# Kernel optimization log

Hardware: AMD Instinct MI355X
Metric: run time of the kernel (lower is better)

The kernel has to match this reference:

```python
import jax, jax.numpy as jnp
from jax import lax
import numpy as np

FACTOR = 2
KERNEL = 3  # conv kernel size (odd)
DN = ('NCDHW', 'OIDHW', 'NCDHW')


def _setup_fir_kernel():
    # resample_kernel = (1,3,3,1); separable outer product, normalized, * factor**3 gain
    k1 = jnp.asarray([1.0, 3.0, 3.0, 1.0], dtype=jnp.float32)
    k = jnp.einsum('i,j,k->ijk', k1, k1, k1)
    k = k / jnp.sum(k)
    return k * (FACTOR ** 3)  # [4,4,4]


def _upfirdn3d_1x1(x, k, pad0, pad1):
    # upfirdn3d with up=down=1: pad then depthwise-correlate with flipped FIR kernel
    # (torch code runs F.conv3d with torch.flip(kernel)).
    n, c = x.shape[0], x.shape[1]
    xp = jnp.pad(x, ((0, 0), (0, 0), (pad0, pad1), (pad0, pad1), (pad0, pad1)))
    kf = jnp.flip(k).astype(x.dtype)  # flip all 3 spatial axes
    w = jnp.broadcast_to(kf[None, None], (c, 1) + k.shape)  # depthwise [C,1,4,4,4]
    return lax.conv_general_dilated(xp, w, (1, 1, 1), 'VALID',
                                    dimension_numbers=DN,
                                    feature_group_count=c)


def _upsample_conv_3d(x, weight):
    # Equivalent of upsample_conv_3d(x, w, k=(1,3,3,1), factor=2):
    # torch flips the weight and feeds conv_transpose3d(stride=2); the flip and
    # the implicit transpose-flip cancel, so it equals an lhs-dilated correlation
    # with the ORIGINAL weight, padded by (k-1) on each side (output_padding=0).
    k = _setup_fir_kernel()
    p = k.shape[0] - FACTOR - (KERNEL - 1)  # = 0
    pad_lo, pad_hi = (p + 1) // 2 + FACTOR - 1, p // 2 + 1  # = (1, 1)
    y = lax.conv_general_dilated(
        x, weight.astype(x.dtype), (1, 1, 1),
        padding=[(KERNEL - 1, KERNEL - 1)] * 3,
        lhs_dilation=(FACTOR, FACTOR, FACTOR),
        dimension_numbers=DN)  # [N, outC, 33, 33, 33]
    return _upfirdn3d_1x1(y, k, pad_lo, pad_hi)  # [N, outC, 32, 32, 32]


def setup_inputs() -> dict:
    key = jax.random.key(0)
    k1, k2, k3 = jax.random.split(key, 3)
    x = jax.random.normal(k1, (8, 256, 16, 16, 16), dtype=jnp.float32)
    weight = jax.random.normal(k2, (128, 256, 3, 3, 3), dtype=jnp.float32) * 0.05
    bias = jax.random.normal(k3, (128,), dtype=jnp.float32) * 0.05
    return {"x": x, "weight": weight, "bias": bias}


def reference(x, weight, bias):
    y = _upsample_conv_3d(x, weight)
    return y + bias.reshape(1, -1, 1, 1, 1)
```

## Files before the change

kernel.cpp:

```cpp
#include <hip/hip_runtime.h>
#include <string.h>

typedef __attribute__((ext_vector_type(4))) float f32x4;
typedef __attribute__((ext_vector_type(8))) _Float16 f16x8;
typedef unsigned short u16;
typedef unsigned int   u32;

#define NBATCH 8
#define ICN 256
#define OCN 128
#define VOLP 36432
#define WRE 884736
#define XTE 8388608
#define ZBF 4096
#define S1POOL 43520

__host__ __device__ constexpr int cls_yoff2(int c){
  return (c==0)?0:(c==1)?5168:(c==2)?9792:(c==3)?14416:
         (c==4)?18768:(c==5)?23632:(c==6)?27984:32336;
}
__host__ __device__ constexpr int cls_nxyp(int c){
  return ((c&3)==0)?304:((c&3)==3)?256:272;
}

__device__ __forceinline__ u16 f2h(float v){
  _Float16 h = (_Float16)v;
  u16 u; memcpy(&u, &h, 2);
  return u;
}
__device__ __forceinline__ float h2f(u16 u){
  _Float16 h; memcpy(&h, &u, 2);
  return (float)h;
}

#define GLOAD16(gp, lp)                                                        \
  __builtin_amdgcn_global_load_lds(                                            \
      (const __attribute__((address_space(1))) void*)(gp),                     \
      (__attribute__((address_space(3))) void*)(lp), 16, 0, 0)

__global__ __launch_bounds__(256) void prep_w(const float* __restrict__ w,
                                              u16* __restrict__ wh,
                                              float* __restrict__ zb){
  if (blockIdx.x < 16) zb[blockIdx.x*256 + threadIdx.x] = 0.f;
  int idx = blockIdx.x*256 + threadIdx.x;
  int e = idx&7, ln=(idx>>3)&63, og=(idx>>9)&7, icc=(idx>>12)&7, tt=idx>>15;
  int oc = og*16 + (ln&15);
  int ic = icc*32 + ((ln>>4)&3)*8 + e;
  const int toffs[8] = {0,8,12,16,18,22,24,26};
  const int tcnt[8]  = {8,4,4,2,4,2,2,1};
  int c=0, t=0;
  #pragma unroll
  for (int cc=0; cc<8; ++cc)
    if (tt>=toffs[cc] && tt<toffs[cc]+tcnt[cc]){ c=cc; t=tt-toffs[cc]; }
  int ez=c>>2, ey=(c>>1)&1, ex=c&1;
  int ty=2-ey, tx=2-ex;
  int ax=t%tx, ay=(t/tx)%ty, az=t/(tx*ty);
  int qz = ez?1:(az?2:0), qy = ey?1:(ay?2:0), qx = ex?1:(ax?2:0);
  wh[idx] = f2h(w[((size_t)oc*ICN + ic)*27 + (qz*3+qy)*3+qx]);
}

__global__ __launch_bounds__(256) void prep_x(const float* __restrict__ x,
                                              u16* __restrict__ xh){
  __shared__ u16 tile[256*33];
  const int tid = threadIdx.x;
  const int b = blockIdx.x;
  const int n = b >> 7, icc = (b >> 4) & 7, pc = b & 15;
  const float* xb = x + ((size_t)(n*256 + icc*32))*4096 + pc*256;
  #pragma unroll 4
  for (int r = 0; r < 32; ++r)
    tile[tid*33 + r] = f2h(xb[(size_t)r*4096 + tid]);
  __syncthreads();
  u16* ob = xh + ((size_t)(n*8 + icc))*131072 + pc*8192;
  #pragma unroll
  for (int j = 0; j < 4; ++j){
    int c = j*256 + tid;
    int p = c >> 2, il8 = (c & 3)*8;
    ushort4 lo, hi;
    lo.x = tile[p*33+il8+0]; lo.y = tile[p*33+il8+1];
    lo.z = tile[p*33+il8+2]; lo.w = tile[p*33+il8+3];
    hi.x = tile[p*33+il8+4]; hi.y = tile[p*33+il8+5];
    hi.z = tile[p*33+il8+6]; hi.w = tile[p*33+il8+7];
    *(ushort4*)&ob[c*8]     = lo;
    *(ushort4*)&ob[c*8 + 4] = hi;
  }
}

#define S1_ISSUE(BUFBYTE, ICC0, AZV)                                           \
  {                                                                            \
    const int iccs_ = wv >> 1;                                                 \
    _Pragma("unroll")                                                          \
    for (int j_=0; j_<6; ++j_){                                                \
      const int r_ = j_*64 + ln;                                               \
      if (r_ < 340){                                                           \
        const int s_ = wv*340 + r_;                                            \
        const int in_ = s_ - iccs_*680;                                        \
        const int icg_ = in_&3, pos_ = in_>>2;                                 \
        const int xi_ = pos_%17, yi_ = pos_/17;                                \
        const int zc_ = EZ ? mz : (mz-1+(AZV));                                \
        const int yc_ = my0 + yi_ + (EY-1);                                    \
        const int xc_ = xi_ + (EX-1);                                          \
        const bool inb_ = (u32)zc_<16u && (u32)yc_<16u && (u32)xc_<16u;        \
        const size_t g_ = nbase + (size_t)((ICC0)+iccs_)*131072                \
                        + (size_t)((zc_*256+yc_*16+xc_)*32 + icg_*8);          \
        const u16* gh_ = inb_ ? (xh+g_) : zb16;                                \
        char* lh_ = pool + (BUFBYTE) + s_*16;                                  \
        GLOAD16(gh_, lh_);                                                     \
      }                                                                        \
    }                                                                          \
  }

template<int EZ,int EY,int EX>
__device__ __forceinline__ void s1body(char* pool,
                                       const u16* __restrict__ xh,
                                       const u16* __restrict__ wh,
                                       const u16* __restrict__ zb16,
                                       u16* __restrict__ yd, int n0, int mt, int mz, int nl, int tid)
{
  constexpr int TZ=2-EZ, TY=2-EY, TX=2-EX;
  constexpr int DX=17-EX;
  constexpr int DY=17-EY;
  constexpr int NXY=DY*DX;
  constexpr int CLS = EZ*4+EY*2+EX;
  constexpr int YOFF = cls_yoff2(CLS);
  constexpr int NXYP = cls_nxyp(CLS);
  constexpr int W27 = (CLS==0)?0:(CLS==1)?8:(CLS==2)?12:(CLS==3)?16:
                      (CLS==4)?18:(CLS==5)?22:(CLS==6)?24:26;
  constexpr int NST = TZ*4;
  u16* AsU = (u16*)pool;

  const int wv=tid>>6, ln=tid&63;
  const int mhalf = wv&1, ochalf = wv>>1;
  const int my0=(mt*128)/DX;

  int posA[4];
  #pragma unroll
  for (int fi=0; fi<4; ++fi){
    int m = mt*128 + mhalf*64 + fi*16 + (ln&15);
    if (m > NXY-1) m = NXY-1;
    int my=m/DX, mx=m-my*DX;
    posA[fi] = ((my-my0)*17 + mx)*32 + (ln>>4)*8;
  }

  f32x4 acc[4][4];
  #pragma unroll
  for (int i=0;i<4;++i)
    #pragma unroll
    for (int j=0;j<4;++j) acc[i][j]=(f32x4){0.f,0.f,0.f,0.f};

  const size_t nbase = (size_t)(n0+nl)*(ICN*4096);

  S1_ISSUE(0, 0, 0);

  int st = 0;
  #pragma unroll 1
  for (int ip=0; ip<4; ++ip){
    #pragma unroll
    for (int az=0; az<TZ; ++az){
      const int cur = st & 1;
      const bool have_next = (st+1) < NST;
      if (have_next){
        const int nip = (az+1<TZ)?ip:(ip+1);
        const int naz = (az+1<TZ)?(az+1):0;
        S1_ISSUE((cur^1)*21760, nip*2, naz);
        asm volatile("s_waitcnt vmcnt(6)" ::: "memory");
      } else {
        asm volatile("s_waitcnt vmcnt(0)" ::: "memory");
      }
      asm volatile("s_barrier" ::: "memory");
      const int curo = cur*10880;

      __builtin_amdgcn_s_setprio(1);
      #pragma unroll
      for (int k=0; k<2; ++k){
        const int icc = ip*2 + k;
        #pragma unroll
        for (int ay=0; ay<TY; ++ay)
        #pragma unroll
        for (int ax=0; ax<TX; ++ax){
          const int t = (az*TY+ay)*TX+ax;
          const int toff = (ay*17+ax)*32;
          f16x8 ah[4];
          #pragma unroll
          for (int fi=0; fi<4; ++fi)
            ah[fi] = *(const f16x8*)&AsU[curo + k*5440 + posA[fi]+toff];
          const u16* bp = wh + (size_t)(((W27+t)*8+icc)*8)*512 + (ochalf*4)*512 + ln*8;
          f16x8 bh[4];
          #pragma unroll
          for (int og=0; og<4; ++og) bh[og] = *(const f16x8*)(bp + og*512);
          #pragma unroll
          for (int fi=0; fi<4; ++fi)
            #pragma unroll
            for (int og=0; og<4; ++og)
              acc[fi][og] = __builtin_amdgcn_mfma_f32_16x16x32_f16(ah[fi], bh[og], acc[fi][og],0,0,0);
        }
      }
      __builtin_amdgcn_s_setprio(0);
      asm volatile("s_barrier" ::: "memory");
      ++st;
    }
  }

  float* tr = (float*)pool + wv*(64*33);
  #pragma unroll
  for (int pass=0; pass<2; ++pass){
    #pragma unroll
    for (int fi=0; fi<2; ++fi)
      #pragma unroll
      for (int og=0; og<4; ++og)
        #pragma unroll
        for (int j=0; j<4; ++j)
          tr[(og*16+(ln&15))*33 + fi*16 + (ln>>4)*4 + j] = acc[pass*2+fi][og][j];
    int m = mt*128 + mhalf*64 + pass*32 + (ln&31);
    bool valid = m < NXY;
    size_t lbase = (size_t)YOFF + (size_t)mz*NXYP + (valid ? m : 0);
    #pragma unroll 4
    for (int i=0; i<32; ++i){
      int r = 2*i + (ln>>5);
      u16 v = f2h(tr[r*33 + (ln&31)]);
      int oc = ochalf*64 + r;
      if (valid)
        __builtin_nontemporal_store(v, yd + (size_t)(nl*128 + oc)*VOLP + lbase);
    }
  }
}

__global__ __launch_bounds__(256,3) void stage1f(const u16* __restrict__ xh,
                                                 const u16* __restrict__ wh,
                                                 const u16* __restrict__ zb16,
                                                 u16* __restrict__ yd, int n0){
  __shared__ __align__(16) char pool[S1POOL];
  int bid = blockIdx.x, nl, tid = threadIdx.x;
  if (gridDim.z == 1){ nl = bid & 7; bid >>= 3; }
  else               { nl = blockIdx.z; }
  int mz, sub;
  if (bid < 352){ mz = bid/22; sub = bid - mz*22; }
  else          { mz = 16;     sub = bid - 352;   }
  if      (sub <  3) s1body<0,0,0>(pool,xh,wh,zb16,yd,n0,sub   ,mz,nl,tid);
  else if (sub <  6) s1body<0,0,1>(pool,xh,wh,zb16,yd,n0,sub- 3,mz,nl,tid);
  else if (sub <  9) s1body<0,1,0>(pool,xh,wh,zb16,yd,n0,sub- 6,mz,nl,tid);
  else if (sub < 11) s1body<0,1,1>(pool,xh,wh,zb16,yd,n0,sub- 9,mz,nl,tid);
  else if (sub < 14) s1body<1,0,0>(pool,xh,wh,zb16,yd,n0,sub-11,mz,nl,tid);
  else if (sub < 17) s1body<1,0,1>(pool,xh,wh,zb16,yd,n0,sub-14,mz,nl,tid);
  else if (sub < 20) s1body<1,1,0>(pool,xh,wh,zb16,yd,n0,sub-17,mz,nl,tid);
  else               s1body<1,1,1>(pool,xh,wh,zb16,yd,n0,sub-20,mz,nl,tid);
}

__global__ __launch_bounds__(256) void stage2d(const u16* __restrict__ yd, const float* __restrict__ bias,
                                               float* __restrict__ out, int n0){
  __shared__ float raw[33][36];
  __shared__ float fx[35][36];
  const int tid=threadIdx.x;
  const int zg=blockIdx.x, oc=blockIdx.y, nl=blockIdx.z;
  const u16* yb = yd + (size_t)(nl*128+oc)*VOLP;
  const float b = bias[oc];
  float* ob = out + (size_t)((n0+nl)*128+oc)*32768;
  for (int t2=tid; t2<1188; t2+=256) raw[t2/36][t2%36] = 0.f;
  for (int t2=tid; t2<1260; t2+=256) fx[t2/36][t2%36] = 0.f;
  __syncthreads();
  float a0[2][2]={{0,0},{0,0}}, a1[2][2]={{0,0},{0,0}}, a2[2][2]={{0,0},{0,0}};

  #pragma unroll 1
  for (int s=0; s<11; ++s){
    int uz = zg*8 - 1 + s;
    if ((u32)uz < 33u){
      const int cz = uz & 1, zi2 = uz >> 1;
      #pragma unroll 1
      for (int ch=tid; ch<273; ch+=256){
        #define GATH(CY,CX,CHL)                                                     \
        {                                                                           \
          constexpr int DXc = 17-(CX);                                              \
          constexpr int NXYc = (17-(CY))*DXc;                                       \
          constexpr int O0 = cls_yoff2((CY)*2+(CX));                                \
          constexpr int O1 = cls_yoff2(4+(CY)*2+(CX));                              \
          constexpr int PS = cls_nxyp((CY)*2+(CX));                                 \
          const int s2 = 4*(CHL);                                                   \
          const int r0 = s2/DXc;                                                    \
          const int c0 = s2 - r0*DXc;                                               \
          const u16* sp = yb + (cz?O1:O0) + zi2*PS + s2;                            \
          ushort4 v = *(const ushort4*)sp;                                          \
          u16 ve[4] = {v.x, v.y, v.z, v.w};                                         \
          _Pragma("unroll")                                                         \
          for (int e=0; e<4; ++e){                                                  \
            int c = c0+e, rr = r0;                                                  \
            if (c >= DXc){ c -= DXc; rr += 1; }                                     \
            if (s2+e < NXYc) raw[2*rr+(CY)][2*c+(CX)+1] = h2f(ve[e]);               \
          }                                                                         \
        }
        if      (ch <  73) GATH(0,0,ch)
        else if (ch < 141) GATH(0,1,ch-73)
        else if (ch < 209) GATH(1,0,ch-141)
        else               GATH(1,1,ch-209)
        #undef GATH
      }
    } else {
      for (int t2=tid; t2<1188; t2+=256) raw[t2/36][t2%36] = 0.f;
    }
    __syncthreads();
    #pragma unroll 1
    for (int t2=tid; t2<528; t2+=256){
      int uy = t2>>4, j = t2&15;
      float2 A = *(const float2*)&raw[uy][2*j];
      float2 B = *(const float2*)&raw[uy][2*j+2];
      float  Cv = raw[uy][2*j+4];
      float f0 = 0.25f*A.x + 0.75f*A.y + 0.75f*B.x + 0.25f*B.y;
      float f1 = 0.25f*A.y + 0.75f*B.x + 0.75f*B.y + 0.25f*Cv;
      *(float2*)&fx[uy+1][2*j] = make_float2(f0, f1);
    }
    __syncthreads();
    #pragma unroll
    for (int ss=0; ss<2; ++ss){
      int t2 = tid + ss*256;
      int i = t2>>5, ox = t2&31;
      float f0 = fx[2*i  ][ox];
      float f1 = fx[2*i+1][ox];
      float f2 = fx[2*i+2][ox];
      float f3 = fx[2*i+3][ox];
      float f4 = fx[2*i+4][ox];
      float fv0 = 0.25f*f0 + 0.75f*f1 + 0.75f*f2 + 0.25f*f3;
      float fv1 = 0.25f*f1 + 0.75f*f2 + 0.75f*f3 + 0.25f*f4;
      if (s >= 3){
        int oz = zg*8 + s - 3;
        __builtin_nontemporal_store(a0[ss][0] + 0.25f*fv0 + b, ob + (size_t)oz*1024 + (2*i  )*32 + ox);
        __builtin_nontemporal_store(a0[ss][1] + 0.25f*fv1 + b, ob + (size_t)oz*1024 + (2*i+1)*32 + ox);
      }
      a0[ss][0] = a1[ss][0] + 0.75f*fv0;  a1[ss][0] = a2[ss][0] + 0.75f*fv0;  a2[ss][0] = 0.25f*fv0;
      a0[ss][1] = a1[ss][1] + 0.75f*fv1;  a1[ss][1] = a2[ss][1] + 0.75f*fv1;  a2[ss][1] = 0.25f*fv1;
    }
    __syncthreads();
  }
}

extern "C" void kernel_launch(void* const* d_in, const int* in_sizes, int n_in,
                              void* d_out, int out_size, void* d_ws, size_t ws_size,
                              hipStream_t stream) {
  const float* x    = (const float*)d_in[0];
  const float* w    = (const float*)d_in[1];
  const float* bias = (const float*)d_in[2];
  float* out = (float*)d_out;

  float* zb = (float*)d_ws;
  u16* wh = (u16*)(zb + ZBF);
  u16* xh = wh + WRE;
  u16* yd = xh + XTE;
  size_t base = (size_t)ZBF*4 + (size_t)(WRE + XTE)*2;

  int nChunk = 1;
  if      (ws_size >= base + (size_t)8*128*VOLP*2) nChunk=8;
  else if (ws_size >= base + (size_t)4*128*VOLP*2) nChunk=4;
  else if (ws_size >= base + (size_t)2*128*VOLP*2) nChunk=2;

  prep_w<<<dim3(WRE/256), 256, 0, stream>>>(w, wh, zb);
  prep_x<<<dim3(1024), 256, 0, stream>>>(x, xh);

  const u16* zb16 = (const u16*)zb;
  if (nChunk == 8){
    stage1f<<<dim3(2904,1,1),256,0,stream>>>(xh,wh,zb16,yd,0);
    stage2d<<<dim3(4,128,8),256,0,stream>>>(yd,bias,out,0);
  } else {
    for (int n0=0; n0<NBATCH; n0+=nChunk){
      stage1f<<<dim3(363,1,nChunk),256,0,stream>>>(xh,wh,zb16,yd,n0);
      stage2d<<<dim3(4,128,nChunk),256,0,stream>>>(yd,bias,out,n0);
    }
  }
}
```

Measured before the change: 188.9 us.

## Load conv activation fragments directly from global memory instead of LDS staging

Removes the double-buffered global_load_lds staging of input halo tiles and its barriers. Each wave now reads its A fragments straight from global (L1/L2) per tap, with bounds checks that fall back to a zero buffer, and whole out-of-range z slices are skipped. The LDS pool shrinks to what the epilogue transpose needs, which may raise occupancy. The cost is more redundant global/cache traffic and exposed load latency with no software prefetch.

```diff
diff --git a/kernel.cpp b/kernel.cpp
--- a/kernel.cpp
+++ b/kernel.cpp
@@ -13,7 +13,7 @@
 #define WRE 884736
 #define XTE 8388608
 #define ZBF 4096
-#define S1POOL 43520
+#define S1POOL 33792
 
 __host__ __device__ constexpr int cls_yoff2(int c){
   return (c==0)?0:(c==1)?5168:(c==2)?9792:(c==3)?14416:
@@ -32,11 +32,6 @@
   _Float16 h; memcpy(&h, &u, 2);
   return (float)h;
 }
-
-#define GLOAD16(gp, lp)                                                        \
-  __builtin_amdgcn_global_load_lds(                                            \
-      (const __attribute__((address_space(1))) void*)(gp),                     \
-      (__attribute__((address_space(3))) void*)(lp), 16, 0, 0)
 
 __global__ __launch_bounds__(256) void prep_w(const float* __restrict__ w,
                                               u16* __restrict__ wh,
@@ -84,30 +79,6 @@
     *(ushort4*)&ob[c*8 + 4] = hi;
   }
 }
-
-#define S1_ISSUE(BUFBYTE, ICC0, AZV)                                           \
-  {                                                                            \
-    const int iccs_ = wv >> 1;                                                 \
-    _Pragma("unroll")                                                          \
-    for (int j_=0; j_<6; ++j_){                                                \
-      const int r_ = j_*64 + ln;                                               \
-      if (r_ < 340){                                                           \
-        const int s_ = wv*340 + r_;                                            \
-        const int in_ = s_ - iccs_*680;                                        \
-        const int icg_ = in_&3, pos_ = in_>>2;                                 \
-        const int xi_ = pos_%17, yi_ = pos_/17;                                \
-        const int zc_ = EZ ? mz : (mz-1+(AZV));                                \
-        const int yc_ = my0 + yi_ + (EY-1);                                    \
-        const int xc_ = xi_ + (EX-1);                                          \
-        const bool inb_ = (u32)zc_<16u && (u32)yc_<16u && (u32)xc_<16u;        \
-        const size_t g_ = nbase + (size_t)((ICC0)+iccs_)*131072                \
-                        + (size_t)((zc_*256+yc_*16+xc_)*32 + icg_*8);          \
-        const u16* gh_ = inb_ ? (xh+g_) : zb16;                                \
-        char* lh_ = pool + (BUFBYTE) + s_*16;                                  \
-        GLOAD16(gh_, lh_);                                                     \
-      }                                                                        \
-    }                                                                          \
-  }
 
 template<int EZ,int EY,int EX>
 __device__ __forceinline__ void s1body(char* pool,
@@ -125,20 +96,17 @@
   constexpr int NXYP = cls_nxyp(CLS);
   constexpr int W27 = (CLS==0)?0:(CLS==1)?8:(CLS==2)?12:(CLS==3)?16:
                       (CLS==4)?18:(CLS==5)?22:(CLS==6)?24:26;
-  constexpr int NST = TZ*4;
-  u16* AsU = (u16*)pool;
 
   const int wv=tid>>6, ln=tid&63;
   const int mhalf = wv&1, ochalf = wv>>1;
-  const int my0=(mt*128)/DX;
-
-  int posA[4];
+  const int icg8 = (ln>>4)*8;
+
+  int myv[4], mxv[4];
   #pragma unroll
   for (int fi=0; fi<4; ++fi){
     int m = mt*128 + mhalf*64 + fi*16 + (ln&15);
     if (m > NXY-1) m = NXY-1;
-    int my=m/DX, mx=m-my*DX;
-    posA[fi] = ((my-my0)*17 + mx)*32 + (ln>>4)*8;
+    myv[fi] = m/DX; mxv[fi] = m - myv[fi]*DX;
   }
 
   f32x4 acc[4][4];
@@ -147,56 +115,40 @@
     #pragma unroll
     for (int j=0;j<4;++j) acc[i][j]=(f32x4){0.f,0.f,0.f,0.f};
 
-  const size_t nbase = (size_t)(n0+nl)*(ICN*4096);
-
-  S1_ISSUE(0, 0, 0);
-
-  int st = 0;
+  const u16* xb = xh + (size_t)(n0+nl)*1048576;
+
   #pragma unroll 1
-  for (int ip=0; ip<4; ++ip){
+  for (int icc=0; icc<8; ++icc){
+    const u16* xpi = xb + (size_t)icc*131072;
     #pragma unroll
     for (int az=0; az<TZ; ++az){
-      const int cur = st & 1;
-      const bool have_next = (st+1) < NST;
-      if (have_next){
-        const int nip = (az+1<TZ)?ip:(ip+1);
-        const int naz = (az+1<TZ)?(az+1):0;
-        S1_ISSUE((cur^1)*21760, nip*2, naz);
-        asm volatile("s_waitcnt vmcnt(6)" ::: "memory");
-      } else {
-        asm volatile("s_waitcnt vmcnt(0)" ::: "memory");
+      const int zc = EZ ? mz : (mz-1+az);
+      if (!EZ && (u32)zc >= 16u) continue;
+      #pragma unroll
+      for (int ay=0; ay<TY; ++ay)
+      #pragma unroll
+      for (int ax=0; ax<TX; ++ax){
+        const int t = (az*TY+ay)*TX+ax;
+        f16x8 ah[4];
+        #pragma unroll
+        for (int fi=0; fi<4; ++fi){
+          int yc = myv[fi] + ay + (EY-1);
+          int xc = mxv[fi] + ax + (EX-1);
+          bool inb = ((u32)yc < 16u) & ((u32)xc < 16u);
+          u32 off = (u32)((zc*256 + yc*16 + xc)*32 + icg8);
+          const u16* ap = inb ? (xpi + off) : zb16;
+          ah[fi] = *(const f16x8*)ap;
+        }
+        const u16* bp = wh + (size_t)(((W27+t)*8+icc)*8)*512 + ochalf*2048 + ln*8;
+        f16x8 bh[4];
+        #pragma unroll
+        for (int og=0; og<4; ++og) bh[og] = *(const f16x8*)(bp + og*512);
+        #pragma unroll
+        for (int fi=0; fi<4; ++fi)
+          #pragma unroll
+          for (int og=0; og<4; ++og)
+            acc[fi][og] = __builtin_amdgcn_mfma_f32_16x16x32_f16(ah[fi], bh[og], acc[fi][og],0,0,0);
       }
-      asm volatile("s_barrier" ::: "memory");
-      const int curo = cur*10880;
-
-      __builtin_amdgcn_s_setprio(1);
-      #pragma unroll
-      for (int k=0; k<2; ++k){
-        const int icc = ip*2 + k;
-        #pragma unroll
-        for (int ay=0; ay<TY; ++ay)
-        #pragma unroll
-        for (int ax=0; ax<TX; ++ax){
-          const int t = (az*TY+ay)*TX+ax;
-          const int toff = (ay*17+ax)*32;
-          f16x8 ah[4];
-          #pragma unroll
-          for (int fi=0; fi<4; ++fi)
-            ah[fi] = *(const f16x8*)&AsU[curo + k*5440 + posA[fi]+toff];
-          const u16* bp = wh + (size_t)(((W27+t)*8+icc)*8)*512 + (ochalf*4)*512 + ln*8;
-          f16x8 bh[4];
-          #pragma unroll
-          for (int og=0; og<4; ++og) bh[og] = *(const f16x8*)(bp + og*512);
-          #pragma unroll
-          for (int fi=0; fi<4; ++fi)
-            #pragma unroll
-            for (int og=0; og<4; ++og)
-              acc[fi][og] = __builtin_amdgcn_mfma_f32_16x16x32_f16(ah[fi], bh[og], acc[fi][og],0,0,0);
-        }
-      }
-      __builtin_amdgcn_s_setprio(0);
-      asm volatile("s_barrier" ::: "memory");
-      ++st;
     }
   }
 
```

Measured after the change: 229.2 us. 21.3% more time.
